# Kernel optimization log

Hardware: AMD Instinct MI355X
Metric: run time of the kernel (lower is better)

Reference implementation:

```python
import jax, jax.numpy as jnp
import numpy as np

D_MODEL = 1024
NUM_HEADS = 16
HEAD_DIM = D_MODEL // NUM_HEADS


def setup_inputs() -> dict:
    key = jax.random.key(0)
    ks = jax.random.split(key, 5)
    B, S = 4, 2048
    x = jax.random.normal(ks[0], (B, S, D_MODEL), dtype=jnp.float32)
    scale = 1.0 / np.sqrt(D_MODEL)
    qkv_w = jax.random.normal(ks[1], (3 * D_MODEL, D_MODEL), dtype=jnp.float32) * scale
    qkv_b = jnp.zeros((3 * D_MODEL,), dtype=jnp.float32)
    out_w = jax.random.normal(ks[2], (D_MODEL, D_MODEL), dtype=jnp.float32) * scale
    out_b = jnp.zeros((D_MODEL,), dtype=jnp.float32)
    return {"x": x, "qkv_w": qkv_w, "qkv_b": qkv_b, "out_w": out_w, "out_b": out_b}


def reference(x, qkv_w, qkv_b, out_w, out_b):
    B, S, _ = x.shape
    # qkv projection (torch Linear: x @ W.T + b)
    qkv = x @ qkv_w.T + qkv_b  # [B, S, 3*D]
    q, k, v = jnp.split(qkv, 3, axis=-1)
    # [B, H, S, hd]
    q = q.reshape(B, S, NUM_HEADS, HEAD_DIM).transpose(0, 2, 1, 3)
    k = k.reshape(B, S, NUM_HEADS, HEAD_DIM).transpose(0, 2, 1, 3)
    v = v.reshape(B, S, NUM_HEADS, HEAD_DIM).transpose(0, 2, 1, 3)
    scores = jnp.einsum('bhqd,bhkd->bhqk', q, k) / np.sqrt(HEAD_DIM).astype(np.float32)
    attn = jax.nn.softmax(scores, axis=-1)
    context = jnp.einsum('bhqk,bhkd->bhqd', attn, v)  # [B, H, S, hd]
    context = context.transpose(0, 2, 1, 3).reshape(B, S, D_MODEL)
    return context @ out_w.T + out_b
```

## Files before the change

### kernel.cpp

```cpp
#include <hip/hip_runtime.h>
#include <hip/hip_bf16.h>
#include <math.h>

#define D_MODEL 1024
#define NHEADS  16
#define HDIM    64
#define BATCH   4
#define SLEN    2048
#define MROWS   (BATCH * SLEN)
#define QKV_N   (3 * D_MODEL)

typedef __attribute__((ext_vector_type(8))) short bhalf8;
typedef __attribute__((ext_vector_type(4))) float f32x4;

#if __has_builtin(__builtin_amdgcn_exp2f)
#define EXP2(x) __builtin_amdgcn_exp2f(x)
#else
#define EXP2(x) exp2f(x)
#endif

static __device__ __forceinline__ unsigned short f2bf(float f) {
    unsigned int u = __builtin_bit_cast(unsigned int, f);
    unsigned int r = (u + 0x7FFFu + ((u >> 16) & 1u)) >> 16;
    return (unsigned short)r;
}

static __device__ __forceinline__ unsigned int pack_hi16(float lo, float hi) {
    return __builtin_amdgcn_perm(__builtin_bit_cast(unsigned int, hi),
                                 __builtin_bit_cast(unsigned int, lo),
                                 0x07060302u);
}

static __device__ __forceinline__ void load_lds16(const void* g, void* l) {
    __builtin_amdgcn_global_load_lds(
        (const __attribute__((address_space(1))) void*)g,
        (__attribute__((address_space(3))) void*)l, 16, 0, 0);
}

__global__ __launch_bounds__(256) void cast_f32_bf16(
    const float* __restrict__ in, unsigned short* __restrict__ out, int n)
{
    int i = (blockIdx.x * 256 + threadIdx.x) * 4;
    if (i < n) {
        float4 v = *(const float4*)(in + i);
        ushort4 o;
        o.x = f2bf(v.x); o.y = f2bf(v.y); o.z = f2bf(v.z); o.w = f2bf(v.w);
        *(ushort4*)(out + i) = o;
    }
}

template<bool BF16OUT>
__global__ __launch_bounds__(256) void gemm_mfma_bt(
    const unsigned short* __restrict__ A,
    const unsigned short* __restrict__ W,
    const float* __restrict__ bias,
    void* __restrict__ outv,
    int M, int N, int K, int qcols, float qscale)
{
    __shared__ __align__(16) unsigned short As[128 * 32];
    __shared__ __align__(16) unsigned short Bs[128 * 32];

    const int tid  = threadIdx.x;
    const int bm   = blockIdx.y * 128;
    const int bn   = blockIdx.x * 128;
    const int wave = tid >> 6;
    const int lane = tid & 63;
    const int m16  = lane & 15;
    const int quad = lane >> 4;
    const int wm   = (wave & 1) * 64;
    const int wn   = (wave >> 1) * 64;

    const int r0 = tid >> 2;
    const int s0 = tid & 3;
    const int g0 = (s0 - (r0 >> 1)) & 3;
    const int g1 = (s0 - ((r0 + 64) >> 1)) & 3;

    const size_t arow0 = (size_t)(bm + r0) * K + g0 * 8;
    const size_t arow1 = (size_t)(bm + r0 + 64) * K + g1 * 8;
    const size_t brow0 = (size_t)(bn + r0) * K + g0 * 8;
    const size_t brow1 = (size_t)(bn + r0 + 64) * K + g1 * 8;

    f32x4 acc[4][4];
    f32x4 zero = {0.f, 0.f, 0.f, 0.f};
#pragma unroll
    for (int i = 0; i < 4; ++i)
#pragma unroll
        for (int j = 0; j < 4; ++j) acc[i][j] = zero;

    for (int kt = 0; kt < K; kt += 32) {
        __syncthreads();
        load_lds16(A + arow0 + kt, As + tid * 8);
        load_lds16(A + arow1 + kt, As + 2048 + tid * 8);
        load_lds16(W + brow0 + kt, Bs + tid * 8);
        load_lds16(W + brow1 + kt, Bs + 2048 + tid * 8);
        __asm__ volatile("s_waitcnt vmcnt(0)" ::: "memory");
        __syncthreads();

        bhalf8 af[4], bf[4];
#pragma unroll
        for (int i = 0; i < 4; ++i) {
            int ra = wm + i * 16 + m16;
            int sa = (quad + (ra >> 1)) & 3;
            af[i] = *(const bhalf8*)&As[ra * 32 + sa * 8];
        }
#pragma unroll
        for (int j = 0; j < 4; ++j) {
            int rb = wn + j * 16 + m16;
            int sb = (quad + (rb >> 1)) & 3;
            bf[j] = *(const bhalf8*)&Bs[rb * 32 + sb * 8];
        }
#pragma unroll
        for (int i = 0; i < 4; ++i)
#pragma unroll
            for (int j = 0; j < 4; ++j)
                acc[i][j] = __builtin_amdgcn_mfma_f32_16x16x32_bf16(
                    af[i], bf[j], acc[i][j], 0, 0, 0);
    }

    float bj[4], scj[4];
#pragma unroll
    for (int j = 0; j < 4; ++j) {
        int col = bn + wn + j * 16 + m16;
        bj[j]  = bias[col];
        scj[j] = (col < qcols) ? qscale : 1.0f;
    }

#pragma unroll
    for (int i = 0; i < 4; ++i) {
#pragma unroll
        for (int r = 0; r < 4; ++r) {
            size_t row = (size_t)(bm + wm + i * 16 + quad * 4 + r);
            if (BF16OUT) {
                unsigned short* dst = (unsigned short*)outv + row * N + bn + wn;
#pragma unroll
                for (int j = 0; j < 4; ++j)
                    dst[j * 16 + m16] = f2bf((acc[i][j][r] + bj[j]) * scj[j]);
            } else {
                float* dst = (float*)outv + row * N + bn + wn;
#pragma unroll
                for (int j = 0; j < 4; ++j)
                    dst[j * 16 + m16] = (acc[i][j][r] + bj[j]) * scj[j];
            }
        }
    }
}

__global__ __launch_bounds__(256) void transpose_v(
    const unsigned short* __restrict__ qkv, unsigned short* __restrict__ vT)
{
    const int kt = blockIdx.x;
    const int h  = blockIdx.y;
    const int b  = blockIdx.z;
    const int tid = threadIdx.x;

    __shared__ __align__(16) unsigned short Vs[64 * 72];

    {
        const unsigned short* src = qkv
            + (size_t)(b * SLEN + kt * 64 + (tid >> 2)) * QKV_N + 2 * D_MODEL + h * HDIM;
        int c = tid & 3;
        *(uint4*)&Vs[(tid >> 2) * 72 + c * 8]       = *(const uint4*)(src + c * 8);
        *(uint4*)&Vs[(tid >> 2) * 72 + (c + 4) * 8] = *(const uint4*)(src + (c + 4) * 8);
    }
    __syncthreads();

    const int d = tid >> 2;
    const int c = tid & 3;
    unsigned short vals[16];
#pragma unroll
    for (int m = 0; m < 16; ++m) {
        int p = c * 16 + m;
        int k = ((p & 3) << 4) | (p >> 2);
        vals[m] = Vs[k * 72 + d];
    }
    unsigned short* dst = vT
        + ((size_t)((b * NHEADS + h) * HDIM + d)) * SLEN + kt * 64 + c * 16;
    *(uint4*)dst       = *(uint4*)&vals[0];
    *(uint4*)(dst + 8) = *(uint4*)&vals[8];
}

__global__ __launch_bounds__(256, 2) void attn_mfma_kernel(
    const unsigned short* __restrict__ qkv,
    const unsigned short* __restrict__ vT,
    unsigned short* __restrict__ ctx)
{
    const int qt = blockIdx.x;
    const int h  = blockIdx.y;
    const int b  = blockIdx.z;
    const int tid  = threadIdx.x;
    const int wave = tid >> 6;
    const int lane = tid & 63;
    const int m16  = lane & 15;
    const int quad = lane >> 4;

    __shared__ __align__(16) unsigned short K_lds[2][64 * 64];
    __shared__ __align__(16) unsigned short V_lds[2][64 * 64];
    __shared__ __align__(16) unsigned short QP_lds[4 * 64 * 72];

    const int srow  = tid >> 3;
    const int sslot = tid & 7;

    const unsigned short* qbase = qkv + (size_t)(b * SLEN + qt * 256) * QKV_N + h * HDIM;
    const unsigned short* kbase = qkv + (size_t)(b * SLEN) * QKV_N + D_MODEL + h * HDIM;
    const unsigned short* vbase = vT + (size_t)((b * NHEADS + h) * HDIM) * SLEN;

#pragma unroll
    for (int c = 0; c < 8; ++c) {
        int r = c * 32 + srow;
        int g = (sslot - r) & 7;
        load_lds16(qbase + (size_t)r * QKV_N + g * 8, QP_lds + c * 2048 + tid * 8);
    }
    {
#pragma unroll
        for (int c = 0; c < 2; ++c) {
            int r = c * 32 + srow;
            int g = (sslot - r) & 7;
            load_lds16(kbase + (size_t)r * QKV_N + g * 8, &K_lds[0][c * 2048 + tid * 8]);
            load_lds16(vbase + (size_t)r * SLEN + g * 8,  &V_lds[0][c * 2048 + tid * 8]);
        }
    }
    __syncthreads();

    bhalf8 qf[4][2];
#pragma unroll
    for (int qi = 0; qi < 4; ++qi) {
        int rq = wave * 64 + qi * 16 + m16;
#pragma unroll
        for (int ks = 0; ks < 2; ++ks) {
            int slot = (ks * 4 + quad + rq) & 7;
            qf[qi][ks] = *(const bhalf8*)&QP_lds[rq * 64 + slot * 8];
        }
    }
    __syncthreads();

    f32x4 zero = {0.f, 0.f, 0.f, 0.f};
    f32x4 oacc[4][4], oacc_l[4];
#pragma unroll
    for (int qi = 0; qi < 4; ++qi) {
        oacc_l[qi] = zero;
#pragma unroll
        for (int dt = 0; dt < 4; ++dt) oacc[qi][dt] = zero;
    }

    bhalf8 ones;
#pragma unroll
    for (int i = 0; i < 8; ++i) ones[i] = (short)0x3F80;

    unsigned short* P = &QP_lds[wave * (64 * 72)];

    for (int kt = 0; kt < SLEN / 64; ++kt) {
        const int buf = kt & 1;

        if (kt + 1 < SLEN / 64) {
            const unsigned short* kb = kbase + (size_t)((kt + 1) * 64) * QKV_N;
            const unsigned short* vb = vbase + (kt + 1) * 64;
#pragma unroll
            for (int c = 0; c < 2; ++c) {
                int r = c * 32 + srow;
                int g = (sslot - r) & 7;
                load_lds16(kb + (size_t)r * QKV_N + g * 8, &K_lds[buf ^ 1][c * 2048 + tid * 8]);
                load_lds16(vb + (size_t)r * SLEN + g * 8,  &V_lds[buf ^ 1][c * 2048 + tid * 8]);
            }
        }

        bhalf8 kf[2][4];
#pragma unroll
        for (int ks = 0; ks < 2; ++ks)
#pragma unroll
            for (int nt = 0; nt < 4; ++nt) {
                int rk = nt * 16 + m16;
                int slot = (ks * 4 + quad + rk) & 7;
                kf[ks][nt] = *(const bhalf8*)&K_lds[buf][rk * 64 + slot * 8];
            }

#pragma unroll
        for (int qi = 0; qi < 4; ++qi) {
            f32x4 sacc[4];
#pragma unroll
            for (int nt = 0; nt < 4; ++nt) sacc[nt] = zero;
#pragma unroll
            for (int ks = 0; ks < 2; ++ks)
#pragma unroll
                for (int nt = 0; nt < 4; ++nt)
                    sacc[nt] = __builtin_amdgcn_mfma_f32_16x16x32_bf16(
                        qf[qi][ks], kf[ks][nt], sacc[nt], 0, 0, 0);

#pragma unroll
            for (int r = 0; r < 4; ++r) {
                float p0 = EXP2(sacc[0][r]);
                float p1 = EXP2(sacc[1][r]);
                float p2 = EXP2(sacc[2][r]);
                float p3 = EXP2(sacc[3][r]);
                uint2 w;
                w.x = pack_hi16(p0, p1);
                w.y = pack_hi16(p2, p3);
                *(uint2*)&P[(qi * 16 + quad * 4 + r) * 72 + m16 * 4] = w;
            }
        }

        __asm__ volatile("s_waitcnt lgkmcnt(0)" ::: "memory");

        bhalf8 vf[2][4];
#pragma unroll
        for (int ks = 0; ks < 2; ++ks)
#pragma unroll
            for (int dt = 0; dt < 4; ++dt) {
                int rv = dt * 16 + m16;
                int slot = (ks * 4 + quad + rv) & 7;
                vf[ks][dt] = *(const bhalf8*)&V_lds[buf][rv * 64 + slot * 8];
            }

#pragma unroll
        for (int ks = 0; ks < 2; ++ks)
#pragma unroll
            for (int qi = 0; qi < 4; ++qi) {
                bhalf8 pf = *(const bhalf8*)&P[(qi * 16 + m16) * 72 + ks * 32 + quad * 8];
                oacc_l[qi] = __builtin_amdgcn_mfma_f32_16x16x32_bf16(
                    pf, ones, oacc_l[qi], 0, 0, 0);
#pragma unroll
                for (int dt = 0; dt < 4; ++dt)
                    oacc[qi][dt] = __builtin_amdgcn_mfma_f32_16x16x32_bf16(
                        pf, vf[ks][dt], oacc[qi][dt], 0, 0, 0);
            }

        __syncthreads();
    }

#pragma unroll
    for (int qi = 0; qi < 4; ++qi) {
#pragma unroll
        for (int r = 0; r < 4; ++r) {
            float inv = 1.0f / oacc_l[qi][r];
            int row = b * SLEN + qt * 256 + wave * 64 + qi * 16 + quad * 4 + r;
            unsigned short* dst = ctx + (size_t)row * D_MODEL + h * HDIM;
#pragma unroll
            for (int dt = 0; dt < 4; ++dt)
                dst[dt * 16 + m16] = f2bf(oacc[qi][dt][r] * inv);
        }
    }
}

extern "C" void kernel_launch(void* const* d_in, const int* in_sizes, int n_in,
                              void* d_out, int out_size, void* d_ws, size_t ws_size,
                              hipStream_t stream)
{
    const float* x     = (const float*)d_in[0];
    const float* qkv_w = (const float*)d_in[1];
    const float* qkv_b = (const float*)d_in[2];
    const float* out_w = (const float*)d_in[3];
    const float* out_b = (const float*)d_in[4];
    float* out = (float*)d_out;

    unsigned short* xbf  = (unsigned short*)d_ws;
    unsigned short* wqkv = xbf  + (size_t)MROWS * D_MODEL;
    unsigned short* wout = wqkv + (size_t)QKV_N * D_MODEL;
    unsigned short* qkv  = wout + (size_t)D_MODEL * D_MODEL;
    unsigned short* ctx  = qkv  + (size_t)MROWS * QKV_N;
    unsigned short* vTb  = ctx  + (size_t)MROWS * D_MODEL;

    {
        int n;
        n = MROWS * D_MODEL;
        cast_f32_bf16<<<n / 1024, 256, 0, stream>>>(x, xbf, n);
        n = QKV_N * D_MODEL;
        cast_f32_bf16<<<n / 1024, 256, 0, stream>>>(qkv_w, wqkv, n);
        n = D_MODEL * D_MODEL;
        cast_f32_bf16<<<n / 1024, 256, 0, stream>>>(out_w, wout, n);
    }

    const float QSCALE = 0.125f * 1.44269504088896f;

    {
        dim3 grid(QKV_N / 128, MROWS / 128);
        gemm_mfma_bt<true><<<grid, 256, 0, stream>>>(xbf, wqkv, qkv_b, qkv,
                                                     MROWS, QKV_N, D_MODEL,
                                                     D_MODEL, QSCALE);
    }

    {
        dim3 grid(SLEN / 64, NHEADS, BATCH);
        transpose_v<<<grid, 256, 0, stream>>>(qkv, vTb);
    }

    {
        dim3 grid(SLEN / 256, NHEADS, BATCH);
        attn_mfma_kernel<<<grid, 256, 0, stream>>>(qkv, vTb, ctx);
    }

    {
        dim3 grid(D_MODEL / 128, MROWS / 128);
        gemm_mfma_bt<false><<<grid, 256, 0, stream>>>(ctx, wout, out_b, out,
                                                      MROWS, D_MODEL, D_MODEL,
                                                      0, 1.0f);
    }
}
```

Before: 284.7 us.

## Fuse casts, vectorize QKV stores, drop ones-MFMA rowsum, shrink out-GEMM tiles

The three fp32-to-bf16 casts are merged into one launch. The QKV GEMM epilogue packs four bf16 values per store for the Q and K columns. This permutes columns within each 64-wide head, which is harmless because Q and K are permuted identically. The attention kernel no longer runs an MFMA against a ones vector to get the softmax denominator. It accumulates the row sums in scalar registers and reduces them with lane shuffles at the end, removing a fifth of the PV-stage MFMAs in exchange for extra VALU adds and register pressure. The output projection uses 64-row tiles to double the block count and improve CU occupancy.

```diff
diff --git a/kernel.cpp b/kernel.cpp
--- a/kernel.cpp
+++ b/kernel.cpp
@@ -25,6 +25,10 @@
     return (unsigned short)r;
 }
 
+static __device__ __forceinline__ unsigned int pack_bf2(float lo, float hi) {
+    return (unsigned int)f2bf(lo) | ((unsigned int)f2bf(hi) << 16);
+}
+
 static __device__ __forceinline__ unsigned int pack_hi16(float lo, float hi) {
     return __builtin_amdgcn_perm(__builtin_bit_cast(unsigned int, hi),
                                  __builtin_bit_cast(unsigned int, lo),
@@ -37,24 +41,31 @@
         (__attribute__((address_space(3))) void*)l, 16, 0, 0);
 }
 
-__global__ __launch_bounds__(256) void cast_f32_bf16(
-    const float* __restrict__ in, unsigned short* __restrict__ out, int n)
+__global__ __launch_bounds__(256) void cast3_f32_bf16(
+    const float* __restrict__ a, int na,
+    const float* __restrict__ b, int nb,
+    const float* __restrict__ c,
+    unsigned short* __restrict__ oa,
+    unsigned short* __restrict__ ob,
+    unsigned short* __restrict__ oc)
 {
     int i = (blockIdx.x * 256 + threadIdx.x) * 4;
-    if (i < n) {
-        float4 v = *(const float4*)(in + i);
-        ushort4 o;
-        o.x = f2bf(v.x); o.y = f2bf(v.y); o.z = f2bf(v.z); o.w = f2bf(v.w);
-        *(ushort4*)(out + i) = o;
-    }
-}
-
-template<bool BF16OUT>
-__global__ __launch_bounds__(256) void gemm_mfma_bt(
+    const float* src;
+    unsigned short* dst;
+    if (i < na)           { src = a + i;            dst = oa + i; }
+    else if (i < na + nb) { src = b + (i - na);     dst = ob + (i - na); }
+    else                  { src = c + (i - na - nb); dst = oc + (i - na - nb); }
+    float4 v = *(const float4*)src;
+    ushort4 o;
+    o.x = f2bf(v.x); o.y = f2bf(v.y); o.z = f2bf(v.z); o.w = f2bf(v.w);
+    *(ushort4*)dst = o;
+}
+
+__global__ __launch_bounds__(256) void gemm_mfma_qkv(
     const unsigned short* __restrict__ A,
     const unsigned short* __restrict__ W,
     const float* __restrict__ bias,
-    void* __restrict__ outv,
+    unsigned short* __restrict__ out,
     int M, int N, int K, int qcols, float qscale)
 {
     __shared__ __align__(16) unsigned short As[128 * 32];
@@ -125,24 +136,114 @@
         scj[j] = (col < qcols) ? qscale : 1.0f;
     }
 
-#pragma unroll
-    for (int i = 0; i < 4; ++i) {
+    if (bn < 2 * D_MODEL) {
+#pragma unroll
+        for (int i = 0; i < 4; ++i)
+#pragma unroll
+            for (int r = 0; r < 4; ++r) {
+                size_t row = (size_t)(bm + wm + i * 16 + quad * 4 + r);
+                float v0 = (acc[i][0][r] + bj[0]) * scj[0];
+                float v1 = (acc[i][1][r] + bj[1]) * scj[1];
+                float v2 = (acc[i][2][r] + bj[2]) * scj[2];
+                float v3 = (acc[i][3][r] + bj[3]) * scj[3];
+                uint2 w;
+                w.x = pack_bf2(v0, v1);
+                w.y = pack_bf2(v2, v3);
+                *(uint2*)(out + row * N + bn + wn + m16 * 4) = w;
+            }
+    } else {
+#pragma unroll
+        for (int i = 0; i < 4; ++i)
+#pragma unroll
+            for (int r = 0; r < 4; ++r) {
+                size_t row = (size_t)(bm + wm + i * 16 + quad * 4 + r);
+                unsigned short* dst = out + row * N + bn + wn;
+#pragma unroll
+                for (int j = 0; j < 4; ++j)
+                    dst[j * 16 + m16] = f2bf(acc[i][j][r] + bj[j]);
+            }
+    }
+}
+
+__global__ __launch_bounds__(256) void gemm_mfma_out(
+    const unsigned short* __restrict__ A,
+    const unsigned short* __restrict__ W,
+    const float* __restrict__ bias,
+    float* __restrict__ out,
+    int M, int N, int K)
+{
+    __shared__ __align__(16) unsigned short As[64 * 32];
+    __shared__ __align__(16) unsigned short Bs[128 * 32];
+
+    const int tid  = threadIdx.x;
+    const int bm   = blockIdx.y * 64;
+    const int bn   = blockIdx.x * 128;
+    const int wave = tid >> 6;
+    const int lane = tid & 63;
+    const int m16  = lane & 15;
+    const int quad = lane >> 4;
+    const int wm   = (wave & 1) * 32;
+    const int wn   = (wave >> 1) * 64;
+
+    const int r0 = tid >> 2;
+    const int s0 = tid & 3;
+    const int g0 = (s0 - (r0 >> 1)) & 3;
+    const int g1 = (s0 - ((r0 + 64) >> 1)) & 3;
+
+    const size_t arow  = (size_t)(bm + r0) * K + g0 * 8;
+    const size_t brow0 = (size_t)(bn + r0) * K + g0 * 8;
+    const size_t brow1 = (size_t)(bn + r0 + 64) * K + g1 * 8;
+
+    f32x4 acc[2][4];
+    f32x4 zero = {0.f, 0.f, 0.f, 0.f};
+#pragma unroll
+    for (int i = 0; i < 2; ++i)
+#pragma unroll
+        for (int j = 0; j < 4; ++j) acc[i][j] = zero;
+
+    for (int kt = 0; kt < K; kt += 32) {
+        __syncthreads();
+        load_lds16(A + arow + kt,  As + tid * 8);
+        load_lds16(W + brow0 + kt, Bs + tid * 8);
+        load_lds16(W + brow1 + kt, Bs + 2048 + tid * 8);
+        __asm__ volatile("s_waitcnt vmcnt(0)" ::: "memory");
+        __syncthreads();
+
+        bhalf8 af[2], bf[4];
+#pragma unroll
+        for (int i = 0; i < 2; ++i) {
+            int ra = wm + i * 16 + m16;
+            int sa = (quad + (ra >> 1)) & 3;
+            af[i] = *(const bhalf8*)&As[ra * 32 + sa * 8];
+        }
+#pragma unroll
+        for (int j = 0; j < 4; ++j) {
+            int rb = wn + j * 16 + m16;
+            int sb = (quad + (rb >> 1)) & 3;
+            bf[j] = *(const bhalf8*)&Bs[rb * 32 + sb * 8];
+        }
+#pragma unroll
+        for (int i = 0; i < 2; ++i)
+#pragma unroll
+            for (int j = 0; j < 4; ++j)
+                acc[i][j] = __builtin_amdgcn_mfma_f32_16x16x32_bf16(
+                    af[i], bf[j], acc[i][j], 0, 0, 0);
+    }
+
+    float bj[4];
+#pragma unroll
+    for (int j = 0; j < 4; ++j) bj[j] = bias[bn + wn + j * 16 + m16];
+
+#pragma unroll
+    for (int i = 0; i < 2; ++i)
 #pragma unroll
         for (int r = 0; r < 4; ++r) {
             size_t row = (size_t)(bm + wm + i * 16 + quad * 4 + r);
-            if (BF16OUT) {
-                unsigned short* dst = (unsigned short*)outv + row * N + bn + wn;
-#pragma unroll
-                for (int j = 0; j < 4; ++j)
-                    dst[j * 16 + m16] = f2bf((acc[i][j][r] + bj[j]) * scj[j]);
-            } else {
-                float* dst = (float*)outv + row * N + bn + wn;
-#pragma unroll
-                for (int j = 0; j < 4; ++j)
-                    dst[j * 16 + m16] = (acc[i][j][r] + bj[j]) * scj[j];
-            }
-        }
-    }
+            float* dst = out + row * N + bn + wn;
+#pragma unroll
+            for (int j = 0; j < 4; ++j)
+                dst[j * 16 + m16] = acc[i][j][r] + bj[j];
+        }
 }
 
 __global__ __launch_bounds__(256) void transpose_v(
@@ -234,17 +335,15 @@
     __syncthreads();
 
     f32x4 zero = {0.f, 0.f, 0.f, 0.f};
-    f32x4 oacc[4][4], oacc_l[4];
+    f32x4 oacc[4][4];
+    float lacc[4][4];
 #pragma unroll
     for (int qi = 0; qi < 4; ++qi) {
-        oacc_l[qi] = zero;
 #pragma unroll
         for (int dt = 0; dt < 4; ++dt) oacc[qi][dt] = zero;
-    }
-
-    bhalf8 ones;
-#pragma unroll
-    for (int i = 0; i < 8; ++i) ones[i] = (short)0x3F80;
+#pragma unroll
+        for (int r = 0; r < 4; ++r) lacc[qi][r] = 0.f;
+    }
 
     unsigned short* P = &QP_lds[wave * (64 * 72)];
 
@@ -291,6 +390,7 @@
                 float p1 = EXP2(sacc[1][r]);
                 float p2 = EXP2(sacc[2][r]);
                 float p3 = EXP2(sacc[3][r]);
+                lacc[qi][r] += (p0 + p1) + (p2 + p3);
                 uint2 w;
                 w.x = pack_hi16(p0, p1);
                 w.y = pack_hi16(p2, p3);
@@ -315,8 +415,6 @@
 #pragma unroll
             for (int qi = 0; qi < 4; ++qi) {
                 bhalf8 pf = *(const bhalf8*)&P[(qi * 16 + m16) * 72 + ks * 32 + quad * 8];
-                oacc_l[qi] = __builtin_amdgcn_mfma_f32_16x16x32_bf16(
-                    pf, ones, oacc_l[qi], 0, 0, 0);
 #pragma unroll
                 for (int dt = 0; dt < 4; ++dt)
                     oacc[qi][dt] = __builtin_amdgcn_mfma_f32_16x16x32_bf16(
@@ -330,7 +428,12 @@
     for (int qi = 0; qi < 4; ++qi) {
 #pragma unroll
         for (int r = 0; r < 4; ++r) {
-            float inv = 1.0f / oacc_l[qi][r];
+            float l = lacc[qi][r];
+            l += __shfl_xor(l, 1);
+            l += __shfl_xor(l, 2);
+            l += __shfl_xor(l, 4);
+            l += __shfl_xor(l, 8);
+            float inv = 1.0f / l;
             int row = b * SLEN + qt * 256 + wave * 64 + qi * 16 + quad * 4 + r;
             unsigned short* dst = ctx + (size_t)row * D_MODEL + h * HDIM;
 #pragma unroll
@@ -359,22 +462,21 @@
     unsigned short* vTb  = ctx  + (size_t)MROWS * D_MODEL;
 
     {
-        int n;
-        n = MROWS * D_MODEL;
-        cast_f32_bf16<<<n / 1024, 256, 0, stream>>>(x, xbf, n);
-        n = QKV_N * D_MODEL;
-        cast_f32_bf16<<<n / 1024, 256, 0, stream>>>(qkv_w, wqkv, n);
-        n = D_MODEL * D_MODEL;
-        cast_f32_bf16<<<n / 1024, 256, 0, stream>>>(out_w, wout, n);
+        int na = MROWS * D_MODEL;
+        int nb = QKV_N * D_MODEL;
+        int nc = D_MODEL * D_MODEL;
+        int blocks = (na + nb + nc) / 1024;
+        cast3_f32_bf16<<<blocks, 256, 0, stream>>>(x, na, qkv_w, nb, out_w,
+                                                   xbf, wqkv, wout);
     }
 
     const float QSCALE = 0.125f * 1.44269504088896f;
 
     {
         dim3 grid(QKV_N / 128, MROWS / 128);
-        gemm_mfma_bt<true><<<grid, 256, 0, stream>>>(xbf, wqkv, qkv_b, qkv,
-                                                     MROWS, QKV_N, D_MODEL,
-                                                     D_MODEL, QSCALE);
+        gemm_mfma_qkv<<<grid, 256, 0, stream>>>(xbf, wqkv, qkv_b, qkv,
+                                                MROWS, QKV_N, D_MODEL,
+                                                D_MODEL, QSCALE);
     }
 
     {
@@ -388,9 +490,8 @@
     }
 
     {
-        dim3 grid(D_MODEL / 128, MROWS / 128);
-        gemm_mfma_bt<false><<<grid, 256, 0, stream>>>(ctx, wout, out_b, out,
-                                                      MROWS, D_MODEL, D_MODEL,
-                                                      0, 1.0f);
-    }
-}
+        dim3 grid(D_MODEL / 128, MROWS / 64);
+        gemm_mfma_out<<<grid, 256, 0, stream>>>(ctx, wout, out_b, out,
+                                                MROWS, D_MODEL, D_MODEL);
+    }
+}
```

After: 299.8 us. +5.3%, slower.
